# Kernel tuning notes

Hardware: AMD Instinct MI355X
Metric: run time of the kernel (lower is better)

## Reference

```python
import jax, jax.numpy as jnp
import numpy as np

N, F_IN, HID, HEADS, NC, E, NG = 50000, 128, 64, 4, 8, 800000, 512


def setup_inputs() -> dict:
    key = jax.random.key(0)
    ks = jax.random.split(key, 16)
    x = jax.random.normal(ks[0], (N, F_IN), dtype=jnp.float32)
    # edges with src != dst so every node's incoming set is exactly {neighbors, self-loop}
    dst = jax.random.randint(ks[1], (E,), 0, N, dtype=jnp.int64)
    off = jax.random.randint(ks[2], (E,), 1, N, dtype=jnp.int64)
    src = (dst + off) % N
    edge_index = jnp.stack([src, dst])
    batch = jnp.sort(jax.random.randint(ks[3], (N,), 0, NG, dtype=jnp.int64))
    g = 1.0 / np.sqrt(F_IN)
    W1 = jax.random.uniform(ks[4], (F_IN, HEADS * HID), jnp.float32, -g, g)
    att_src1 = jax.random.normal(ks[5], (HEADS, HID), jnp.float32) * 0.1
    att_dst1 = jax.random.normal(ks[6], (HEADS, HID), jnp.float32) * 0.1
    b1 = jnp.zeros((HEADS * HID,), jnp.float32)
    g2 = 1.0 / np.sqrt(HEADS * HID)
    W2 = jax.random.uniform(ks[7], (HEADS * HID, HID), jnp.float32, -g2, g2)
    att_src2 = jax.random.normal(ks[8], (1, HID), jnp.float32) * 0.1
    att_dst2 = jax.random.normal(ks[9], (1, HID), jnp.float32) * 0.1
    b2 = jnp.zeros((HID,), jnp.float32)
    g3 = 1.0 / np.sqrt(HID)
    lin_w = jax.random.uniform(ks[10], (HID, NC), jnp.float32, -g3, g3)
    lin_b = jnp.zeros((NC,), jnp.float32)
    return dict(x=x, edge_index=edge_index, batch=batch, W1=W1, att_src1=att_src1,
                att_dst1=att_dst1, b1=b1, W2=W2, att_src2=att_src2, att_dst2=att_dst2,
                b2=b2, lin_w=lin_w, lin_b=lin_b)


def gat_layer(x, src, dst, W, att_s, att_d, bias, heads, out_ch):
    # PyG GATConv: h = x @ W, e_ij = LeakyReLU(a_s.h_j + a_d.h_i), softmax over dst groups
    h = (x @ W).reshape(-1, heads, out_ch)                    # [N,H,C]
    a_s = jnp.einsum('nhc,hc->nh', h, att_s)                  # [N,H]
    a_d = jnp.einsum('nhc,hc->nh', h, att_d)
    e = jax.nn.leaky_relu(a_s[src] + a_d[dst], 0.2)           # [Ef,H]
    m = jax.ops.segment_max(e, dst, num_segments=N)           # stable segment softmax
    ex = jnp.exp(e - m[dst])
    s = jax.ops.segment_sum(ex, dst, num_segments=N)
    alpha = ex / (s[dst] + 1e-16)                             # [Ef,H]
    msg = h[src] * alpha[:, :, None]                          # [Ef,H,C]
    out = jax.ops.segment_sum(msg, dst, num_segments=N)       # [N,H,C]
    return out.reshape(-1, heads * out_ch) + bias, alpha


def reference(x, edge_index, batch, W1, att_src1, att_dst1, b1,
              W2, att_src2, att_dst2, b2, lin_w, lin_b):
    loops = jnp.arange(N, dtype=edge_index.dtype)
    src = jnp.concatenate([edge_index[0], loops])             # add self-loops (PyG default)
    dst = jnp.concatenate([edge_index[1], loops])
    h, alpha1 = gat_layer(x, src, dst, W1, att_src1, att_dst1, b1, HEADS, HID)
    h = jax.nn.relu(h)
    # conv2 on edge_index_1 (already has self-loops; PyG remove+add is a no-op here)
    h, alpha2 = gat_layer(h, src, dst, W2, att_src2, att_dst2, b2, 1, HID)
    h = jax.nn.relu(h)
    sums = jax.ops.segment_sum(h, batch, num_segments=NG)     # global_mean_pool
    cnt = jax.ops.segment_sum(jnp.ones((N,), h.dtype), batch, num_segments=NG)
    pooled = sums / jnp.maximum(cnt, 1.0)[:, None]
    # dropout is identity in eval mode
    return pooled @ lin_w + lin_b
```

## Files before the change

kernel.cpp:

```cpp
#include <hip/hip_runtime.h>

#define F_IN 128
#define HID 64
#define HEADS 4
#define NC 8

typedef __bf16 bf16_t;
typedef bf16_t bf16x8 __attribute__((ext_vector_type(8)));
typedef float f32x4 __attribute__((ext_vector_type(4)));

union BF8 { bf16x8 v; ushort u[8]; };


__device__ __forceinline__ ushort f2bf(float f) {
    uint u = __float_as_uint(f);
    return (ushort)((u + 0x7fffu + ((u >> 16) & 1u)) >> 16);
}
__device__ __forceinline__ float bf2f(ushort h) {
    return __uint_as_float(((uint)h) << 16);
}
__device__ __forceinline__ float edgew(float e) {
    e = (e > 0.f) ? e : 0.2f * e;
    return __expf(e);
}

__global__ void k_setup(const float* __restrict__ W1, const float* __restrict__ W2,
                        ushort* __restrict__ w1hi,
                        ushort* __restrict__ w2hi, ushort* __restrict__ w2lo,
                        int* __restrict__ deg, int N, int* __restrict__ counts, int NG) {
    int i = blockIdx.x * blockDim.x + threadIdx.x;
    if (i < N) deg[i] = 1;
    if (i < NG) counts[i] = 0;
    if (i < 128 * 256) {
        int k = i >> 8, n = i & 255;
        int cy = n >> 7, ct = (n >> 4) & 7, c = n & 15, kc = k >> 5, ls = (k >> 3) & 3, j = k & 7;
        size_t off = ((((size_t)cy * 8 + ct) * 4 + kc) * 64 + (ls * 16 + c)) * 8 + j;
        w1hi[off] = f2bf(W1[i]);
    }
    if (i < 256 * 64) {
        int k = i >> 6, n = i & 63;
        int ct = n >> 4, c = n & 15, kc = k >> 5, ls = (k >> 3) & 3, j = k & 7;
        size_t off = (((size_t)ct * 8 + kc) * 64 + (ls * 16 + c)) * 8 + j;
        float w = W2[i];
        ushort hi = f2bf(w);
        w2hi[off] = hi; w2lo[off] = f2bf(w - bf2f(hi));
    }
}

__global__ void k_count(const int* __restrict__ ei, int E, int* __restrict__ deg,
                        const int* __restrict__ batch, int N, int* __restrict__ counts) {
    int i = blockIdx.x * blockDim.x + threadIdx.x;
    if (i < E) atomicAdd(&deg[ei[E + i]], 1);
    if (i < N) atomicAdd(&counts[batch[i]], 1);
}

__global__ __launch_bounds__(1024) void k_scan_part(const int* __restrict__ v,
                                                    int* __restrict__ excl,
                                                    int* __restrict__ bsum, int n) {
    __shared__ int buf[1024];
    int tid = threadIdx.x;
    int i = blockIdx.x * 1024 + tid;
    int val = (i < n) ? v[i] : 0;
    buf[tid] = val;
    __syncthreads();
    for (int off = 1; off < 1024; off <<= 1) {
        int t = (tid >= off) ? buf[tid - off] : 0;
        __syncthreads();
        buf[tid] += t;
        __syncthreads();
    }
    if (i < n) excl[i] = buf[tid] - val;
    if (tid == 1023) bsum[blockIdx.x] = buf[1023];
}

__global__ __launch_bounds__(1024) void k_scan_small2(const int* __restrict__ bsum,
                                                      int* __restrict__ boff, int nb,
                                                      int* __restrict__ total_out,
                                                      const int* __restrict__ counts,
                                                      int* __restrict__ gstart, int ng) {
    __shared__ int buf[1024];
    int tid = threadIdx.x;
    const int* src = (blockIdx.x == 0) ? bsum : counts;
    int cnt = (blockIdx.x == 0) ? nb : ng;
    int val = (tid < cnt) ? src[tid] : 0;
    buf[tid] = val;
    __syncthreads();
    for (int off = 1; off < 1024; off <<= 1) {
        int t = (tid >= off) ? buf[tid - off] : 0;
        __syncthreads();
        buf[tid] += t;
        __syncthreads();
    }
    if (blockIdx.x == 0) {
        if (tid < cnt) boff[tid] = buf[tid] - val;
        if (tid == 1023) total_out[0] = buf[1023];
    } else {
        if (tid < cnt) gstart[tid] = buf[tid] - val;
        if (tid == 1023) gstart[ng] = buf[1023];
    }
}

__global__ void k_scan_add_self(int* __restrict__ rowstart, const int* __restrict__ boff,
                                int* __restrict__ cursor, int* __restrict__ csr, int n) {
    int i = blockIdx.x * blockDim.x + threadIdx.x;
    if (i < n) {
        int rs = rowstart[i] + boff[i >> 10];
        rowstart[i] = rs;
        csr[rs] = i;
        cursor[i] = 1;
    }
}

__global__ void k_scatter(const int* __restrict__ ei, int E, const int* __restrict__ rowstart,
                          int* __restrict__ cursor, int* __restrict__ csr) {
    int e = blockIdx.x * blockDim.x + threadIdx.x;
    if (e < E) {
        int d = ei[E + e], s = ei[e];
        int pos = atomicAdd(&cursor[d], 1);
        csr[rowstart[d] + pos] = s;
    }
}

__global__ __launch_bounds__(256) void k_gemm1(const float* __restrict__ x,
                                               const ushort* __restrict__ w1hi,
                                               const float* __restrict__ atts,
                                               const float* __restrict__ attd,
                                               ushort* __restrict__ h1b,
                                               float* __restrict__ as1, float* __restrict__ ad1,
                                               int N) {
    __shared__ __align__(16) ushort lhi[16384];
    int tid = threadIdx.x;
    int cy = blockIdx.y;
    {
        float4* dh = (float4*)lhi; const float4* sh = (const float4*)(w1hi + (size_t)cy * 16384);
        #pragma unroll
        for (int i = 0; i < 8; i++) dh[tid + i * 256] = sh[tid + i * 256];
    }
    __syncthreads();
    int w = tid >> 6, l = tid & 63;
    int lc = l & 15, lk = l >> 4;
    int rbase = blockIdx.x * 256 + w * 64;

    f32x4 acc[4][8];
    #pragma unroll
    for (int mt = 0; mt < 4; mt++)
        #pragma unroll
        for (int ct = 0; ct < 8; ct++) acc[mt][ct] = (f32x4){0.f, 0.f, 0.f, 0.f};

    #pragma unroll
    for (int kc = 0; kc < 4; kc++) {
        BF8 ahi[4], alo[4];
        #pragma unroll
        for (int mt = 0; mt < 4; mt++) {
            int row = rbase + mt * 16 + lc;
            float4 v0 = {0.f, 0.f, 0.f, 0.f}, v1 = v0;
            if (row < N) {
                const float* xp = x + (size_t)row * F_IN + kc * 32 + lk * 8;
                v0 = *(const float4*)xp; v1 = *(const float4*)(xp + 4);
            }
            float vals[8] = {v0.x, v0.y, v0.z, v0.w, v1.x, v1.y, v1.z, v1.w};
            #pragma unroll
            for (int j = 0; j < 8; j++) {
                ushort h = f2bf(vals[j]);
                ahi[mt].u[j] = h;
                alo[mt].u[j] = f2bf(vals[j] - bf2f(h));
            }
        }
        #pragma unroll
        for (int ct = 0; ct < 8; ct++) {
            int boff = ((ct * 4 + kc) * 64 + l) * 8;
            bf16x8 bhi = *(const bf16x8*)(lhi + boff);
            #pragma unroll
            for (int mt = 0; mt < 4; mt++) {
                acc[mt][ct] = __builtin_amdgcn_mfma_f32_16x16x32_bf16(ahi[mt].v, bhi, acc[mt][ct], 0, 0, 0);
                acc[mt][ct] = __builtin_amdgcn_mfma_f32_16x16x32_bf16(alo[mt].v, bhi, acc[mt][ct], 0, 0, 0);
            }
        }
    }
    #pragma unroll
    for (int mt = 0; mt < 4; mt++) {
        int rowb = rbase + mt * 16 + lk * 4;
        #pragma unroll
        for (int ct = 0; ct < 8; ct++) {
            int col = cy * 128 + ct * 16 + lc;
            #pragma unroll
            for (int r = 0; r < 4; r++) {
                int row = rowb + r;
                if (row < N) h1b[(size_t)row * 256 + col] = f2bf(acc[mt][ct][r]);
            }
        }
        #pragma unroll
        for (int hh = 0; hh < 2; hh++) {
            float s[4] = {0.f, 0.f, 0.f, 0.f}, d[4] = {0.f, 0.f, 0.f, 0.f};
            #pragma unroll
            for (int cq = 0; cq < 4; cq++) {
                int ct = hh * 4 + cq;
                int col = cy * 128 + ct * 16 + lc;
                float av = atts[col], dv = attd[col];
                #pragma unroll
                for (int r = 0; r < 4; r++) { s[r] += acc[mt][ct][r] * av; d[r] += acc[mt][ct][r] * dv; }
            }
            #pragma unroll
            for (int r = 0; r < 4; r++) {
                #pragma unroll
                for (int off = 1; off < 16; off <<= 1) {
                    s[r] += __shfl_xor(s[r], off);
                    d[r] += __shfl_xor(d[r], off);
                }
            }
            if (lc == 0) {
                int head = cy * 2 + hh;
                #pragma unroll
                for (int r = 0; r < 4; r++) {
                    int row = rowb + r;
                    if (row < N) { as1[row * 4 + head] = s[r]; ad1[row * 4 + head] = d[r]; }
                }
            }
        }
    }
}

__global__ __launch_bounds__(256) void k_gemm2(const ushort* __restrict__ xin,
                                               const ushort* __restrict__ w2hi,
                                               const ushort* __restrict__ w2lo,
                                               const float* __restrict__ atts,
                                               const float* __restrict__ attd,
                                               ushort* __restrict__ h2b,
                                               float* __restrict__ as2, float* __restrict__ ad2,
                                               int N) {
    __shared__ __align__(16) ushort lhi[16384];
    __shared__ __align__(16) ushort llo[16384];
    int tid = threadIdx.x;
    {
        float4* dh = (float4*)lhi; const float4* sh = (const float4*)w2hi;
        float4* dl = (float4*)llo; const float4* sl = (const float4*)w2lo;
        #pragma unroll
        for (int i = 0; i < 8; i++) {
            dh[tid + i * 256] = sh[tid + i * 256];
            dl[tid + i * 256] = sl[tid + i * 256];
        }
    }
    __syncthreads();
    int w = tid >> 6, l = tid & 63;
    int lc = l & 15, lk = l >> 4;
    int rbase = blockIdx.x * 256 + w * 64;

    f32x4 acc[4][4];
    #pragma unroll
    for (int mt = 0; mt < 4; mt++)
        #pragma unroll
        for (int ct = 0; ct < 4; ct++) acc[mt][ct] = (f32x4){0.f, 0.f, 0.f, 0.f};

    #pragma unroll
    for (int kc = 0; kc < 8; kc++) {
        BF8 a[4];
        #pragma unroll
        for (int mt = 0; mt < 4; mt++) {
            int row = rbase + mt * 16 + lc;
            if (row < N) {
                a[mt].v = *(const bf16x8*)(xin + (size_t)row * 256 + kc * 32 + lk * 8);
            } else {
                #pragma unroll
                for (int j = 0; j < 8; j++) a[mt].u[j] = 0;
            }
        }
        #pragma unroll
        for (int ct = 0; ct < 4; ct++) {
            int boff = ((ct * 8 + kc) * 64 + l) * 8;
            bf16x8 bhi = *(const bf16x8*)(lhi + boff);
            bf16x8 blo = *(const bf16x8*)(llo + boff);
            #pragma unroll
            for (int mt = 0; mt < 4; mt++) {
                acc[mt][ct] = __builtin_amdgcn_mfma_f32_16x16x32_bf16(a[mt].v, bhi, acc[mt][ct], 0, 0, 0);
                acc[mt][ct] = __builtin_amdgcn_mfma_f32_16x16x32_bf16(a[mt].v, blo, acc[mt][ct], 0, 0, 0);
            }
        }
    }
    #pragma unroll
    for (int mt = 0; mt < 4; mt++) {
        int rowb = rbase + mt * 16 + lk * 4;
        #pragma unroll
        for (int ct = 0; ct < 4; ct++) {
            int col = ct * 16 + lc;
            #pragma unroll
            for (int r = 0; r < 4; r++) {
                int row = rowb + r;
                if (row < N) h2b[(size_t)row * 64 + col] = f2bf(acc[mt][ct][r]);
            }
        }
        float s[4] = {0.f, 0.f, 0.f, 0.f}, d[4] = {0.f, 0.f, 0.f, 0.f};
        #pragma unroll
        for (int ct = 0; ct < 4; ct++) {
            int col = ct * 16 + lc;
            float av = atts[col], dv = attd[col];
            #pragma unroll
            for (int r = 0; r < 4; r++) { s[r] += acc[mt][ct][r] * av; d[r] += acc[mt][ct][r] * dv; }
        }
        #pragma unroll
        for (int r = 0; r < 4; r++) {
            #pragma unroll
            for (int off = 1; off < 16; off <<= 1) {
                s[r] += __shfl_xor(s[r], off);
                d[r] += __shfl_xor(d[r], off);
            }
        }
        if (lc == 0) {
            #pragma unroll
            for (int r = 0; r < 4; r++) {
                int row = rowb + r;
                if (row < N) { as2[row] = s[r]; ad2[row] = d[r]; }
            }
        }
    }
}


__global__ __launch_bounds__(256) void k_edgew1(const int* __restrict__ rowstart,
                                                const int* __restrict__ csr,
                                                const float* __restrict__ as1,
                                                const float* __restrict__ ad1,
                                                float* __restrict__ w4,
                                                float* __restrict__ issum1, int N) {
    int n = blockIdx.x * 4 + (threadIdx.x >> 6);
    int lane = threadIdx.x & 63;
    if (n >= N) return;
    int beg = rowstart[n], end = rowstart[n + 1];
    float4 adv = *(const float4*)(ad1 + (size_t)n * 4);
    float s0 = 0.f, s1 = 0.f, s2 = 0.f, s3 = 0.f;
    for (int jb = beg; jb < end; jb += 64) {
        int j = jb + lane;
        if (j < end) {
            int s = csr[j];
            float4 av = *(const float4*)(as1 + (size_t)s * 4);
            float w0 = edgew(av.x + adv.x);
            float w1 = edgew(av.y + adv.y);
            float w2 = edgew(av.z + adv.z);
            float w3 = edgew(av.w + adv.w);
            float4 wv = {w0, w1, w2, w3};
            *(float4*)(w4 + (size_t)j * 4) = wv;
            s0 += w0; s1 += w1; s2 += w2; s3 += w3;
        }
    }
    #pragma unroll
    for (int off = 32; off > 0; off >>= 1) {
        s0 += __shfl_xor(s0, off); s1 += __shfl_xor(s1, off);
        s2 += __shfl_xor(s2, off); s3 += __shfl_xor(s3, off);
    }
    if (lane == 0) {
        float4 iv = {1.f / s0, 1.f / s1, 1.f / s2, 1.f / s3};
        *(float4*)(issum1 + (size_t)n * 4) = iv;
    }
}

__global__ __launch_bounds__(256) void k_edgew2(const int* __restrict__ rowstart,
                                                const int* __restrict__ csr,
                                                const float* __restrict__ as2,
                                                const float* __restrict__ ad2,
                                                float* __restrict__ w2a,
                                                float* __restrict__ issum2, int N) {
    int n = blockIdx.x * 4 + (threadIdx.x >> 6);
    int lane = threadIdx.x & 63;
    if (n >= N) return;
    int beg = rowstart[n], end = rowstart[n + 1];
    float adv = ad2[n];
    float ss = 0.f;
    for (int jb = beg; jb < end; jb += 64) {
        int j = jb + lane;
        if (j < end) {
            int s = csr[j];
            float w = edgew(as2[s] + adv);
            w2a[j] = w;
            ss += w;
        }
    }
    #pragma unroll
    for (int off = 32; off > 0; off >>= 1) ss += __shfl_xor(ss, off);
    if (lane == 0) issum2[n] = 1.f / ss;
}


__global__ __launch_bounds__(256) void k_agg1(const ushort* __restrict__ h1b,
                                              const float* __restrict__ w4,
                                              const float* __restrict__ issum1,
                                              const int* __restrict__ rowstart, const int* __restrict__ csr,
                                              const float* __restrict__ b1,
                                              ushort* __restrict__ out1b, int N) {
    int n = blockIdx.x * 4 + (threadIdx.x >> 6);
    int lane = threadIdx.x & 63;
    if (n >= N) return;
    int head = lane >> 4;
    int coff = lane * 4;
    int beg = rowstart[n], end = rowstart[n + 1];
    float inv = issum1[(size_t)n * 4 + head];
    float a0 = 0.f, a1 = 0.f, a2 = 0.f, a3 = 0.f;
    int j = beg;
    for (; j + 8 <= end; j += 8) {
        int s[8]; float wv[8]; ushort4 hv[8];
        #pragma unroll
        for (int i = 0; i < 8; i++) s[i] = csr[j + i];
        #pragma unroll
        for (int i = 0; i < 8; i++) wv[i] = w4[(size_t)(j + i) * 4 + head];
        #pragma unroll
        for (int i = 0; i < 8; i++) hv[i] = *(const ushort4*)(h1b + (size_t)s[i] * 256 + coff);
        #pragma unroll
        for (int i = 0; i < 8; i++) {
            a0 += wv[i] * bf2f(hv[i].x); a1 += wv[i] * bf2f(hv[i].y);
            a2 += wv[i] * bf2f(hv[i].z); a3 += wv[i] * bf2f(hv[i].w);
        }
    }
    for (; j < end; j++) {
        int s0 = csr[j];
        float wv = w4[(size_t)j * 4 + head];
        ushort4 v0 = *(const ushort4*)(h1b + (size_t)s0 * 256 + coff);
        a0 += wv * bf2f(v0.x); a1 += wv * bf2f(v0.y);
        a2 += wv * bf2f(v0.z); a3 += wv * bf2f(v0.w);
    }
    float o0 = fmaxf(a0 * inv + b1[coff + 0], 0.f);
    float o1 = fmaxf(a1 * inv + b1[coff + 1], 0.f);
    float o2 = fmaxf(a2 * inv + b1[coff + 2], 0.f);
    float o3 = fmaxf(a3 * inv + b1[coff + 3], 0.f);
    ushort4 o;
    o.x = f2bf(o0); o.y = f2bf(o1); o.z = f2bf(o2); o.w = f2bf(o3);
    *(ushort4*)(out1b + (size_t)n * 256 + coff) = o;
}

__global__ __launch_bounds__(256) void k_agg2(const ushort* __restrict__ h2b,
                                              const float* __restrict__ w2a,
                                              const float* __restrict__ issum2,
                                              const int* __restrict__ rowstart, const int* __restrict__ csr,
                                              const float* __restrict__ b2,
                                              float* __restrict__ out2, int N) {
    int n = blockIdx.x * 4 + (threadIdx.x >> 6);
    int lane = threadIdx.x & 63;
    if (n >= N) return;
    int g = lane >> 4, li = lane & 15;
    int coff = li * 4;
    int beg = rowstart[n], end = rowstart[n + 1];
    float a0 = 0.f, a1 = 0.f, a2 = 0.f, a3 = 0.f;
    int j = beg;
    for (; j + 8 <= end; j += 8) {
        int sA = csr[j + g], sB = csr[j + 4 + g];
        float wA = w2a[j + g], wB = w2a[j + 4 + g];
        ushort4 hA = *(const ushort4*)(h2b + (size_t)sA * 64 + coff);
        ushort4 hB = *(const ushort4*)(h2b + (size_t)sB * 64 + coff);
        a0 += wA * bf2f(hA.x) + wB * bf2f(hB.x);
        a1 += wA * bf2f(hA.y) + wB * bf2f(hB.y);
        a2 += wA * bf2f(hA.z) + wB * bf2f(hB.z);
        a3 += wA * bf2f(hA.w) + wB * bf2f(hB.w);
    }
    {
        int j1 = j + g, j2 = j + 4 + g;
        if (j1 < end) {
            int s = csr[j1]; float wv = w2a[j1];
            ushort4 hv = *(const ushort4*)(h2b + (size_t)s * 64 + coff);
            a0 += wv * bf2f(hv.x); a1 += wv * bf2f(hv.y);
            a2 += wv * bf2f(hv.z); a3 += wv * bf2f(hv.w);
        }
        if (j2 < end) {
            int s = csr[j2]; float wv = w2a[j2];
            ushort4 hv = *(const ushort4*)(h2b + (size_t)s * 64 + coff);
            a0 += wv * bf2f(hv.x); a1 += wv * bf2f(hv.y);
            a2 += wv * bf2f(hv.z); a3 += wv * bf2f(hv.w);
        }
    }
    a0 += __shfl_xor(a0, 16); a0 += __shfl_xor(a0, 32);
    a1 += __shfl_xor(a1, 16); a1 += __shfl_xor(a1, 32);
    a2 += __shfl_xor(a2, 16); a2 += __shfl_xor(a2, 32);
    a3 += __shfl_xor(a3, 16); a3 += __shfl_xor(a3, 32);
    if (g == 0) {
        float inv = issum2[n];
        float4 o;
        o.x = fmaxf(a0 * inv + b2[coff + 0], 0.f);
        o.y = fmaxf(a1 * inv + b2[coff + 1], 0.f);
        o.z = fmaxf(a2 * inv + b2[coff + 2], 0.f);
        o.w = fmaxf(a3 * inv + b2[coff + 3], 0.f);
        *(float4*)(out2 + (size_t)n * 64 + coff) = o;
    }
}


__global__ __launch_bounds__(64) void k_pool(const float* __restrict__ out2,
                                             const int* __restrict__ gstart,
                                             const float* __restrict__ lin_w,
                                             const float* __restrict__ lin_b,
                                             float* __restrict__ out, int NG) {
    __shared__ float mean[64];
    int g = blockIdx.x;
    int lane = threadIdx.x;
    int beg = gstart[g], end = gstart[g + 1];
    float s = 0.f;
    for (int n = beg; n < end; n++) s += out2[(size_t)n * 64 + lane];
    float cnt = (float)(end - beg);
    mean[lane] = s / fmaxf(cnt, 1.f);
    __syncthreads();
    if (lane < NC) {
        float acc = lin_b[lane];
        #pragma unroll
        for (int c = 0; c < 64; c++) acc += mean[c] * lin_w[c * NC + lane];
        out[g * NC + lane] = acc;
    }
}


extern "C" void kernel_launch(void* const* d_in, const int* in_sizes, int n_in,
                              void* d_out, int out_size, void* d_ws, size_t ws_size,
                              hipStream_t stream) {
    const float* x      = (const float*)d_in[0];
    const int*   ei     = (const int*)d_in[1];
    const int*   batch  = (const int*)d_in[2];
    const float* W1     = (const float*)d_in[3];
    const float* att_s1 = (const float*)d_in[4];
    const float* att_d1 = (const float*)d_in[5];
    const float* b1     = (const float*)d_in[6];
    const float* W2     = (const float*)d_in[7];
    const float* att_s2 = (const float*)d_in[8];
    const float* att_d2 = (const float*)d_in[9];
    const float* b2     = (const float*)d_in[10];
    const float* lin_w  = (const float*)d_in[11];
    const float* lin_b  = (const float*)d_in[12];
    float* out = (float*)d_out;

    const int N  = in_sizes[0] / F_IN;
    const int E  = in_sizes[1] / 2;
    const int NG = out_size / NC;
    const int NE = E + N;
    const int NB = (N + 1023) / 1024;

    char* p = (char*)d_ws;
    auto alloc = [&](size_t bytes) { char* r = p; p += (bytes + 255) & ~(size_t)255; return r; };
    ushort* h1b     = (ushort*)alloc(sizeof(ushort) * (size_t)N * 256);
    ushort* out1b   = (ushort*)alloc(sizeof(ushort) * (size_t)N * 256);
    ushort* h2b     = (ushort*)alloc(sizeof(ushort) * (size_t)N * 64);
    float*  out2    = (float*)alloc(sizeof(float) * (size_t)N * 64);
    float*  as1     = (float*)alloc(sizeof(float) * (size_t)N * 4);
    float*  ad1     = (float*)alloc(sizeof(float) * (size_t)N * 4);
    float*  as2     = (float*)alloc(sizeof(float) * (size_t)N);
    float*  ad2     = (float*)alloc(sizeof(float) * (size_t)N);
    float*  w4      = (float*)alloc(sizeof(float) * (size_t)NE * 4);
    float*  w2a     = (float*)alloc(sizeof(float) * (size_t)NE);
    float*  issum1  = (float*)alloc(sizeof(float) * (size_t)N * 4);
    float*  issum2  = (float*)alloc(sizeof(float) * (size_t)N);
    int*    rowstart= (int*)alloc(sizeof(int) * (size_t)(N + 1));
    int*    itmp    = (int*)alloc(sizeof(int) * (size_t)N);
    int*    csr     = (int*)alloc(sizeof(int) * (size_t)NE);
    int*    counts  = (int*)alloc(sizeof(int) * (size_t)NG);
    int*    gstart  = (int*)alloc(sizeof(int) * (size_t)(NG + 1));
    int*    bsum    = (int*)alloc(sizeof(int) * 1024);
    int*    boff    = (int*)alloc(sizeof(int) * 1024);
    ushort* w1hi    = (ushort*)alloc(sizeof(ushort) * 32768);
    ushort* w2hi    = (ushort*)alloc(sizeof(ushort) * 16384);
    ushort* w2lo    = (ushort*)alloc(sizeof(ushort) * 16384);

    int bs = 256;
    k_setup<<<(N + bs - 1) / bs, bs, 0, stream>>>(W1, W2, w1hi, w2hi, w2lo,
                                                  itmp, N, counts, NG);
    k_count<<<(E + bs - 1) / bs, bs, 0, stream>>>(ei, E, itmp, batch, N, counts);
    k_scan_part<<<NB, 1024, 0, stream>>>(itmp, rowstart, bsum, N);
    k_scan_small2<<<2, 1024, 0, stream>>>(bsum, boff, NB, rowstart + N, counts, gstart, NG);
    k_scan_add_self<<<(N + 1023) / 1024, 1024, 0, stream>>>(rowstart, boff, itmp, csr, N);
    k_scatter<<<(E + bs - 1) / bs, bs, 0, stream>>>(ei, E, rowstart, itmp, csr);

    k_gemm1<<<dim3((N + 255) / 256, 2), 256, 0, stream>>>(x, w1hi, att_s1, att_d1, h1b, as1, ad1, N);
    k_edgew1<<<(N + 3) / 4, 256, 0, stream>>>(rowstart, csr, as1, ad1, w4, issum1, N);
    k_agg1<<<(N + 3) / 4, 256, 0, stream>>>(h1b, w4, issum1, rowstart, csr, b1, out1b, N);

    k_gemm2<<<(N + 255) / 256, 256, 0, stream>>>(out1b, w2hi, w2lo, att_s2, att_d2, h2b, as2, ad2, N);
    k_edgew2<<<(N + 3) / 4, 256, 0, stream>>>(rowstart, csr, as2, ad2, w2a, issum2, N);
    k_agg2<<<(N + 3) / 4, 256, 0, stream>>>(h2b, w2a, issum2, rowstart, csr, b2, out2, N);

    k_pool<<<NG, 64, 0, stream>>>(out2, gstart, lin_w, lin_b, out, NG);
}
```

Baseline: 327.9 us.

## Split aggregation into column slices across blocks and transpose edge weights

Both aggregation kernels are restructured so each node's features are split into 8 column slices, each handled by a separate block. Within a wave, lanes are spread over edges rather than feature columns and partial sums are combined with cross-lane shuffles. The layer-1 edge weights are stored head-major so each slice reads one contiguous weight stream. The goal is more parallelism per node and wider 16-byte gathers. In exchange there are 8x more blocks, and rowstart and csr are read redundantly once per slice. Because the average degree is about 17, many lanes sit idle in layer 2, where one wave spans 64 edges.

```diff
diff --git a/kernel.cpp b/kernel.cpp
--- a/kernel.cpp
+++ b/kernel.cpp
@@ -314,13 +314,12 @@
     }
 }
 
-
 __global__ __launch_bounds__(256) void k_edgew1(const int* __restrict__ rowstart,
                                                 const int* __restrict__ csr,
                                                 const float* __restrict__ as1,
                                                 const float* __restrict__ ad1,
-                                                float* __restrict__ w4,
-                                                float* __restrict__ issum1, int N) {
+                                                float* __restrict__ wT,
+                                                float* __restrict__ issum1, int N, int NE) {
     int n = blockIdx.x * 4 + (threadIdx.x >> 6);
     int lane = threadIdx.x & 63;
     if (n >= N) return;
@@ -336,8 +335,10 @@
             float w1 = edgew(av.y + adv.y);
             float w2 = edgew(av.z + adv.z);
             float w3 = edgew(av.w + adv.w);
-            float4 wv = {w0, w1, w2, w3};
-            *(float4*)(w4 + (size_t)j * 4) = wv;
+            wT[j] = w0;
+            wT[(size_t)NE + j] = w1;
+            wT[(size_t)2 * NE + j] = w2;
+            wT[(size_t)3 * NE + j] = w3;
             s0 += w0; s1 += w1; s2 += w2; s3 += w3;
         }
     }
@@ -379,102 +380,120 @@
 }
 
 
-__global__ __launch_bounds__(256) void k_agg1(const ushort* __restrict__ h1b,
-                                              const float* __restrict__ w4,
-                                              const float* __restrict__ issum1,
-                                              const int* __restrict__ rowstart, const int* __restrict__ csr,
-                                              const float* __restrict__ b1,
-                                              ushort* __restrict__ out1b, int N) {
-    int n = blockIdx.x * 4 + (threadIdx.x >> 6);
-    int lane = threadIdx.x & 63;
+__global__ __launch_bounds__(256) void k_csagg1(const ushort* __restrict__ h1b,
+                                                const float* __restrict__ wT,
+                                                const float* __restrict__ issum1,
+                                                const int* __restrict__ rowstart,
+                                                const int* __restrict__ csr,
+                                                const float* __restrict__ b1,
+                                                ushort* __restrict__ out1b, int N, int NE) {
+    int slice = blockIdx.x & 7;
+    int nb = blockIdx.x >> 3;
+    int wid = threadIdx.x >> 6, lane = threadIdx.x & 63;
+    int n = nb * 4 + wid;
     if (n >= N) return;
-    int head = lane >> 4;
-    int coff = lane * 4;
+    int head = slice >> 1;
+    int e = lane >> 2, sub = lane & 3;
+    int cbase = slice * 32 + sub * 8;
     int beg = rowstart[n], end = rowstart[n + 1];
-    float inv = issum1[(size_t)n * 4 + head];
-    float a0 = 0.f, a1 = 0.f, a2 = 0.f, a3 = 0.f;
-    int j = beg;
-    for (; j + 8 <= end; j += 8) {
-        int s[8]; float wv[8]; ushort4 hv[8];
-        #pragma unroll
-        for (int i = 0; i < 8; i++) s[i] = csr[j + i];
-        #pragma unroll
-        for (int i = 0; i < 8; i++) wv[i] = w4[(size_t)(j + i) * 4 + head];
-        #pragma unroll
-        for (int i = 0; i < 8; i++) hv[i] = *(const ushort4*)(h1b + (size_t)s[i] * 256 + coff);
-        #pragma unroll
-        for (int i = 0; i < 8; i++) {
-            a0 += wv[i] * bf2f(hv[i].x); a1 += wv[i] * bf2f(hv[i].y);
-            a2 += wv[i] * bf2f(hv[i].z); a3 += wv[i] * bf2f(hv[i].w);
-        }
-    }
-    for (; j < end; j++) {
-        int s0 = csr[j];
-        float wv = w4[(size_t)j * 4 + head];
-        ushort4 v0 = *(const ushort4*)(h1b + (size_t)s0 * 256 + coff);
-        a0 += wv * bf2f(v0.x); a1 += wv * bf2f(v0.y);
-        a2 += wv * bf2f(v0.z); a3 += wv * bf2f(v0.w);
-    }
-    float o0 = fmaxf(a0 * inv + b1[coff + 0], 0.f);
-    float o1 = fmaxf(a1 * inv + b1[coff + 1], 0.f);
-    float o2 = fmaxf(a2 * inv + b1[coff + 2], 0.f);
-    float o3 = fmaxf(a3 * inv + b1[coff + 3], 0.f);
-    ushort4 o;
-    o.x = f2bf(o0); o.y = f2bf(o1); o.z = f2bf(o2); o.w = f2bf(o3);
-    *(ushort4*)(out1b + (size_t)n * 256 + coff) = o;
-}
-
-__global__ __launch_bounds__(256) void k_agg2(const ushort* __restrict__ h2b,
-                                              const float* __restrict__ w2a,
-                                              const float* __restrict__ issum2,
-                                              const int* __restrict__ rowstart, const int* __restrict__ csr,
-                                              const float* __restrict__ b2,
-                                              float* __restrict__ out2, int N) {
-    int n = blockIdx.x * 4 + (threadIdx.x >> 6);
-    int lane = threadIdx.x & 63;
+    const float* wp = wT + (size_t)head * NE;
+    float a[8];
+    #pragma unroll
+    for (int i = 0; i < 8; i++) a[i] = 0.f;
+    for (int j0 = beg; j0 < end; j0 += 16) {
+        int j = j0 + e;
+        if (j < end) {
+            int src = csr[j];
+            float w = wp[j];
+            uint4 hv = *(const uint4*)(h1b + (size_t)src * 256 + cbase);
+            a[0] += w * bf2f((ushort)(hv.x & 0xffffu));
+            a[1] += w * bf2f((ushort)(hv.x >> 16));
+            a[2] += w * bf2f((ushort)(hv.y & 0xffffu));
+            a[3] += w * bf2f((ushort)(hv.y >> 16));
+            a[4] += w * bf2f((ushort)(hv.z & 0xffffu));
+            a[5] += w * bf2f((ushort)(hv.z >> 16));
+            a[6] += w * bf2f((ushort)(hv.w & 0xffffu));
+            a[7] += w * bf2f((ushort)(hv.w >> 16));
+        }
+    }
+    #pragma unroll
+    for (int i = 0; i < 8; i++) {
+        a[i] += __shfl_xor(a[i], 4);
+        a[i] += __shfl_xor(a[i], 8);
+        a[i] += __shfl_xor(a[i], 16);
+        a[i] += __shfl_xor(a[i], 32);
+    }
+    if (e == 0) {
+        float inv = issum1[(size_t)n * 4 + head];
+        const float4* bv = (const float4*)(b1 + cbase);
+        float4 bA = bv[0], bB = bv[1];
+        float o0 = fmaxf(a[0] * inv + bA.x, 0.f), o1 = fmaxf(a[1] * inv + bA.y, 0.f);
+        float o2 = fmaxf(a[2] * inv + bA.z, 0.f), o3 = fmaxf(a[3] * inv + bA.w, 0.f);
+        float o4 = fmaxf(a[4] * inv + bB.x, 0.f), o5 = fmaxf(a[5] * inv + bB.y, 0.f);
+        float o6 = fmaxf(a[6] * inv + bB.z, 0.f), o7 = fmaxf(a[7] * inv + bB.w, 0.f);
+        uint4 ov;
+        ov.x = (uint)f2bf(o0) | ((uint)f2bf(o1) << 16);
+        ov.y = (uint)f2bf(o2) | ((uint)f2bf(o3) << 16);
+        ov.z = (uint)f2bf(o4) | ((uint)f2bf(o5) << 16);
+        ov.w = (uint)f2bf(o6) | ((uint)f2bf(o7) << 16);
+        *(uint4*)(out1b + (size_t)n * 256 + cbase) = ov;
+    }
+}
+
+__global__ __launch_bounds__(256) void k_csagg2(const ushort* __restrict__ h2b,
+                                                const float* __restrict__ w2a,
+                                                const float* __restrict__ issum2,
+                                                const int* __restrict__ rowstart,
+                                                const int* __restrict__ csr,
+                                                const float* __restrict__ b2,
+                                                float* __restrict__ out2, int N) {
+    int slice = blockIdx.x & 7;
+    int nb = blockIdx.x >> 3;
+    int wid = threadIdx.x >> 6, lane = threadIdx.x & 63;
+    int n = nb * 4 + wid;
     if (n >= N) return;
-    int g = lane >> 4, li = lane & 15;
-    int coff = li * 4;
+    int cbase = slice * 8;
     int beg = rowstart[n], end = rowstart[n + 1];
-    float a0 = 0.f, a1 = 0.f, a2 = 0.f, a3 = 0.f;
-    int j = beg;
-    for (; j + 8 <= end; j += 8) {
-        int sA = csr[j + g], sB = csr[j + 4 + g];
-        float wA = w2a[j + g], wB = w2a[j + 4 + g];
-        ushort4 hA = *(const ushort4*)(h2b + (size_t)sA * 64 + coff);
-        ushort4 hB = *(const ushort4*)(h2b + (size_t)sB * 64 + coff);
-        a0 += wA * bf2f(hA.x) + wB * bf2f(hB.x);
-        a1 += wA * bf2f(hA.y) + wB * bf2f(hB.y);
-        a2 += wA * bf2f(hA.z) + wB * bf2f(hB.z);
-        a3 += wA * bf2f(hA.w) + wB * bf2f(hB.w);
-    }
-    {
-        int j1 = j + g, j2 = j + 4 + g;
-        if (j1 < end) {
-            int s = csr[j1]; float wv = w2a[j1];
-            ushort4 hv = *(const ushort4*)(h2b + (size_t)s * 64 + coff);
-            a0 += wv * bf2f(hv.x); a1 += wv * bf2f(hv.y);
-            a2 += wv * bf2f(hv.z); a3 += wv * bf2f(hv.w);
-        }
-        if (j2 < end) {
-            int s = csr[j2]; float wv = w2a[j2];
-            ushort4 hv = *(const ushort4*)(h2b + (size_t)s * 64 + coff);
-            a0 += wv * bf2f(hv.x); a1 += wv * bf2f(hv.y);
-            a2 += wv * bf2f(hv.z); a3 += wv * bf2f(hv.w);
-        }
-    }
-    a0 += __shfl_xor(a0, 16); a0 += __shfl_xor(a0, 32);
-    a1 += __shfl_xor(a1, 16); a1 += __shfl_xor(a1, 32);
-    a2 += __shfl_xor(a2, 16); a2 += __shfl_xor(a2, 32);
-    a3 += __shfl_xor(a3, 16); a3 += __shfl_xor(a3, 32);
-    if (g == 0) {
+    float a[8];
+    #pragma unroll
+    for (int i = 0; i < 8; i++) a[i] = 0.f;
+    for (int j0 = beg; j0 < end; j0 += 64) {
+        int j = j0 + lane;
+        if (j < end) {
+            int src = csr[j];
+            float w = w2a[j];
+            uint4 hv = *(const uint4*)(h2b + (size_t)src * 64 + cbase);
+            a[0] += w * bf2f((ushort)(hv.x & 0xffffu));
+            a[1] += w * bf2f((ushort)(hv.x >> 16));
+            a[2] += w * bf2f((ushort)(hv.y & 0xffffu));
+            a[3] += w * bf2f((ushort)(hv.y >> 16));
+            a[4] += w * bf2f((ushort)(hv.z & 0xffffu));
+            a[5] += w * bf2f((ushort)(hv.z >> 16));
+            a[6] += w * bf2f((ushort)(hv.w & 0xffffu));
+            a[7] += w * bf2f((ushort)(hv.w >> 16));
+        }
+    }
+    #pragma unroll
+    for (int i = 0; i < 8; i++) {
+        a[i] += __shfl_xor(a[i], 1);
+        a[i] += __shfl_xor(a[i], 2);
+        a[i] += __shfl_xor(a[i], 4);
+        a[i] += __shfl_xor(a[i], 8);
+        a[i] += __shfl_xor(a[i], 16);
+        a[i] += __shfl_xor(a[i], 32);
+    }
+    if (lane == 0) {
         float inv = issum2[n];
-        float4 o;
-        o.x = fmaxf(a0 * inv + b2[coff + 0], 0.f);
-        o.y = fmaxf(a1 * inv + b2[coff + 1], 0.f);
-        o.z = fmaxf(a2 * inv + b2[coff + 2], 0.f);
-        o.w = fmaxf(a3 * inv + b2[coff + 3], 0.f);
-        *(float4*)(out2 + (size_t)n * 64 + coff) = o;
+        const float4* bv = (const float4*)(b2 + cbase);
+        float4 bA = bv[0], bB = bv[1];
+        float4 oA, oB;
+        oA.x = fmaxf(a[0] * inv + bA.x, 0.f); oA.y = fmaxf(a[1] * inv + bA.y, 0.f);
+        oA.z = fmaxf(a[2] * inv + bA.z, 0.f); oA.w = fmaxf(a[3] * inv + bA.w, 0.f);
+        oB.x = fmaxf(a[4] * inv + bB.x, 0.f); oB.y = fmaxf(a[5] * inv + bB.y, 0.f);
+        oB.z = fmaxf(a[6] * inv + bB.z, 0.f); oB.w = fmaxf(a[7] * inv + bB.w, 0.f);
+        float* op = out2 + (size_t)n * 64 + cbase;
+        *(float4*)op = oA;
+        *(float4*)(op + 4) = oB;
     }
 }
 
@@ -536,7 +555,7 @@
     float*  ad1     = (float*)alloc(sizeof(float) * (size_t)N * 4);
     float*  as2     = (float*)alloc(sizeof(float) * (size_t)N);
     float*  ad2     = (float*)alloc(sizeof(float) * (size_t)N);
-    float*  w4      = (float*)alloc(sizeof(float) * (size_t)NE * 4);
+    float*  wT      = (float*)alloc(sizeof(float) * (size_t)NE * 4);
     float*  w2a     = (float*)alloc(sizeof(float) * (size_t)NE);
     float*  issum1  = (float*)alloc(sizeof(float) * (size_t)N * 4);
     float*  issum2  = (float*)alloc(sizeof(float) * (size_t)N);
@@ -561,12 +580,12 @@
     k_scatter<<<(E + bs - 1) / bs, bs, 0, stream>>>(ei, E, rowstart, itmp, csr);
 
     k_gemm1<<<dim3((N + 255) / 256, 2), 256, 0, stream>>>(x, w1hi, att_s1, att_d1, h1b, as1, ad1, N);
-    k_edgew1<<<(N + 3) / 4, 256, 0, stream>>>(rowstart, csr, as1, ad1, w4, issum1, N);
-    k_agg1<<<(N + 3) / 4, 256, 0, stream>>>(h1b, w4, issum1, rowstart, csr, b1, out1b, N);
+    k_edgew1<<<(N + 3) / 4, 256, 0, stream>>>(rowstart, csr, as1, ad1, wT, issum1, N, NE);
+    k_csagg1<<<((N + 3) / 4) * 8, 256, 0, stream>>>(h1b, wT, issum1, rowstart, csr, b1, out1b, N, NE);
 
     k_gemm2<<<(N + 255) / 256, 256, 0, stream>>>(out1b, w2hi, w2lo, att_s2, att_d2, h2b, as2, ad2, N);
     k_edgew2<<<(N + 3) / 4, 256, 0, stream>>>(rowstart, csr, as2, ad2, w2a, issum2, N);
-    k_agg2<<<(N + 3) / 4, 256, 0, stream>>>(h2b, w2a, issum2, rowstart, csr, b2, out2, N);
+    k_csagg2<<<((N + 3) / 4) * 8, 256, 0, stream>>>(h2b, w2a, issum2, rowstart, csr, b2, out2, N);
 
     k_pool<<<NG, 64, 0, stream>>>(out2, gstart, lin_w, lin_b, out, NG);
 }
```

Result: slower. 585.8 us (+78.7%).
